# Optimization experiments

Hardware: AMD Instinct MI355X
Metric: run time of the kernel (lower is better)

The kernel has to match this reference:

```python
import jax, jax.numpy as jnp
import numpy as np

SCALE = 4.0  # InputEmbedding scale
D = 16       # coordinate dim (InputEmbedding input_dim)


def _p(k, shape, s=0.05):
    return jax.random.normal(k, shape, dtype=jnp.float32) * s


def setup_inputs() -> dict:
    key = jax.random.key(0)
    ks = jax.random.split(key, 20)
    T, N, E, H = 8, 2048, 256, 768
    return {
        "observed": jax.random.normal(ks[0], (T, N, D), dtype=jnp.float32),
        "emb_W": _p(ks[1], (E, D)), "emb_b": _p(ks[2], (E,)),
        "e1_Wih": _p(ks[3], (3 * H, E)), "e1_Whh": _p(ks[4], (3 * H, H)),
        "e1_bih": _p(ks[5], (3 * H,)), "e1_bhh": _p(ks[6], (3 * H,)),
        "e2_Wih": _p(ks[7], (3 * H, E + H)), "e2_Whh": _p(ks[8], (3 * H, H)),
        "e2_bih": _p(ks[9], (3 * H,)), "e2_bhh": _p(ks[10], (3 * H,)),
        "dec_Wih": _p(ks[11], (3 * H, E)), "dec_Whh": _p(ks[12], (3 * H, H)),
        "dec_bih": _p(ks[13], (3 * H,)), "dec_bhh": _p(ks[14], (3 * H,)),
        "h2n_W": _p(ks[15], (5, H)), "h2n_b": _p(ks[16], (5,)),
        "mix_W": _p(ks[17], (D, 5)), "mix_b": _p(ks[18], (D,)),
        "n_predict": 12,
    }


def _gru(x, h, Wih, Whh, bih, bhh):
    # torch.nn.GRUCell math
    gi = x @ Wih.T + bih          # [N, 3H]
    gh = h @ Whh.T + bhh          # [N, 3H]
    ir, iz, in_ = jnp.split(gi, 3, axis=-1)
    hr, hz, hn = jnp.split(gh, 3, axis=-1)
    r = jax.nn.sigmoid(ir + hr)
    z = jax.nn.sigmoid(iz + hz)
    n = jnp.tanh(in_ + r * hn)
    return (1.0 - z) * n + z * h


def reference(observed, emb_W, emb_b,
              e1_Wih, e1_Whh, e1_bih, e1_bhh,
              e2_Wih, e2_Whh, e2_bih, e2_bhh,
              dec_Wih, dec_Whh, dec_bih, dec_bhh,
              h2n_W, h2n_b, mix_W, mix_b, n_predict):
    T, N, _ = observed.shape
    H = e1_Whh.shape[1]
    embed = lambda v: (SCALE * v) @ emb_W.T + emb_b   # InputEmbedding
    h0 = jnp.zeros((N, H), observed.dtype)

    # --- backward (inverse-time) encoder1 pass ---
    inv = observed[::-1]
    vel_b = inv[:-1] - inv[1:]          # obs2 - obs1 on reversed sequence, [T-1, N, D]
    def step1(h, v):
        return _gru(embed(v), h, e1_Wih, e1_Whh, e1_bih, e1_bhh), None
    h_inv, _ = jax.lax.scan(step1, h0, vel_b)
    # NOTE: original mutates the python hidden_state list in place, so every
    # h_invs entry aliases the FINAL encoder1 state -> h_inv is constant over t.

    # --- forward encoder2 pass (input = [embed(vel), h_inv]) ---
    vel_f = observed[1:] - observed[:-1]   # [T-1, N, D]
    def step2(h, v):
        x = jnp.concatenate([embed(v), h_inv], axis=1)
        return _gru(x, h, e2_Wih, e2_Whh, e2_bih, e2_bhh), None
    h, _ = jax.lax.scan(step2, h0, vel_f)

    def h2n(hs):
        # Hidden2Normal: linear then constrain sigmas / correlation
        n = hs @ h2n_W.T + h2n_b
        return jnp.concatenate(
            [n[:, :2], 0.01 + 0.2 * jax.nn.softplus(n[:, 2:4]), 0.7 * jnp.tanh(n[:, 4:5])],
            axis=1)

    def dec_step(h, obs1, obs2):
        h = _gru(embed(obs2 - obs1), h, dec_Wih, dec_Whh, dec_bih, dec_bhh)
        normal = h2n(h)                                   # [N, 5]
        pos = obs2 + jax.nn.relu(normal @ mix_W.T + mix_b)  # mix: Linear(5 -> 16)
        return h, normal, pos

    # decoder step i=0: (observed[-2], observed[-1]); i=1: (observed[-1], positions[-1].detach())
    h, n0, p0 = dec_step(h, observed[-2], observed[-1])
    h, n1, p1 = dec_step(h, observed[-1], jax.lax.stop_gradient(p0))

    def scan_step(carry, _):
        h, pm2, pm1 = carry
        h, n, p = dec_step(h, jax.lax.stop_gradient(pm2), jax.lax.stop_gradient(pm1))
        return (h, pm1, p), (n, p)
    _, (ns, ps) = jax.lax.scan(scan_step, (h, p0, p1), None, length=n_predict - 2)

    rel_pred_scene = jnp.concatenate([jnp.stack([n0, n1]), ns], axis=0)  # [n_predict, N, 5]
    pred_scene = jnp.concatenate([jnp.stack([p0, p1]), ps], axis=0)      # [n_predict, N, 16]
    return rel_pred_scene, pred_scene
```

## Files before the change

### kernel.cpp

```cpp
#include <hip/hip_runtime.h>
#include <hip/hip_bf16.h>
#include <math.h>

#define H 768
#define NB 2048
#define DD 16

typedef __attribute__((ext_vector_type(8))) short bf16x8;
typedef __attribute__((ext_vector_type(4))) float f32x4;

__device__ __forceinline__ void gload_lds16(const void* g, void* lds) {
  __builtin_amdgcn_global_load_lds((const __attribute__((address_space(1))) void*)g,
                                   (__attribute__((address_space(3))) void*)lds, 16, 0, 0);
}
__device__ __forceinline__ float b2f(short s) {
  union { unsigned int u; float f; } c;
  c.u = ((unsigned int)(unsigned short)s) << 16;
  return c.f;
}
__device__ __forceinline__ short f2bs(float f) {
  __hip_bfloat16 h = __float2bfloat16(f);
  return *(short*)&h;
}

__global__ void k_m1(const float* __restrict__ e1W, const float* __restrict__ e2W,
                     const float* __restrict__ dW, const float* __restrict__ embW,
                     float* __restrict__ M1) {
  int idx = blockIdx.x * 256 + threadIdx.x;
  if (idx >= 3 * 2304 * 16) return;
  int d = idx & 15, g = (idx >> 4) % 2304, s = idx / (2304 * 16);
  const float* W = s == 0 ? e1W : s == 1 ? e2W : dW;
  int ld = s == 1 ? 1024 : 256;
  float sum = 0.f;
  for (int e = 0; e < 256; ++e) sum += W[(size_t)g * ld + e] * embW[e * 16 + d];
  M1[idx] = 4.0f * sum;
}

__global__ void k_biasP(const float* __restrict__ e1W, const float* __restrict__ e2W,
                        const float* __restrict__ dW, const float* __restrict__ embB,
                        const float* b1i, const float* b1h, const float* b2i, const float* b2h,
                        const float* b3i, const float* b3h, float* __restrict__ out) {
  int idx = blockIdx.x * 256 + threadIdx.x;
  if (idx >= 3 * 3072) return;
  int c = idx % 3072, s = idx / 3072;
  int f = (c >> 4) & 3, u = (c >> 6) * 16 + (c & 15);
  const float* W = s == 0 ? e1W : s == 1 ? e2W : dW;
  int ld = s == 1 ? 1024 : 256;
  const float* bi = s == 0 ? b1i : s == 1 ? b2i : b3i;
  const float* bh = s == 0 ? b1h : s == 1 ? b2h : b3h;
  float v;
  if (f == 3) {
    v = bh[1536 + u];
  } else {
    int g = (f < 2 ? f * 768 : 1536) + u;
    float acc = bi[g] + (f < 2 ? bh[g] : 0.f);
    for (int e = 0; e < 256; ++e) acc += W[(size_t)g * ld + e] * embB[e];
    v = acc;
  }
  out[idx] = v;
}

__global__ void k_packB3(const float* __restrict__ W1, const float* __restrict__ W2,
                         const float* __restrict__ W3, const float* __restrict__ M1all,
                         __hip_bfloat16* __restrict__ B1, __hip_bfloat16* __restrict__ B2,
                         __hip_bfloat16* __restrict__ B3) {
  int idx = blockIdx.x * 256 + threadIdx.x;
  if (idx >= 3072 * 800) return;
  int s = blockIdx.y;
  const float* Whh = s == 0 ? W1 : s == 1 ? W2 : W3;
  const float* M1s = M1all + (size_t)s * 2304 * 16;
  __hip_bfloat16* Bp = s == 0 ? B1 : s == 1 ? B2 : B3;
  int k = idx % 800, c = idx / 800;
  int f = (c >> 4) & 3, u = (c >> 6) * 16 + (c & 15);
  float v = 0.f;
  if (k < 768) {
    if (f == 0) v = Whh[(size_t)u * 768 + k];
    else if (f == 1) v = Whh[(size_t)(768 + u) * 768 + k];
    else if (f == 3) v = Whh[(size_t)(1536 + u) * 768 + k];
  } else if (k < 784) {
    if (f < 3) v = M1s[(size_t)(f * 768 + u) * 16 + (k - 768)];
  }
  Bp[idx] = __float2bfloat16(v);
}

__global__ void k_packB2g(const float* __restrict__ e2W, __hip_bfloat16* __restrict__ B2g) {
  int idx = blockIdx.x * 256 + threadIdx.x;
  if (idx >= 3072 * 768) return;
  int k = idx % 768, c = idx / 768;
  int f = (c >> 4) & 3, u = (c >> 6) * 16 + (c & 15);
  float v = (f < 3) ? e2W[(size_t)(f * 768 + u) * 1024 + 256 + k] : 0.f;
  B2g[idx] = __float2bfloat16(v);
}

__global__ void k_vel(const float* __restrict__ obs, __hip_bfloat16* __restrict__ velall) {
  int idx = blockIdx.x * 256 + threadIdx.x;
  if (idx >= 7 * 2048 * 32) return;
  int d = idx & 31, n = (idx >> 5) & 2047, s = idx >> 16;
  float v = 0.f;
  if (d < 16)
    v = obs[((size_t)(s + 1) * NB + n) * DD + d] - obs[((size_t)s * NB + n) * DD + d];
  velall[idx] = __float2bfloat16(v);
}

__global__ __launch_bounds__(256) void k_plain(
    const __hip_bfloat16* __restrict__ A, const __hip_bfloat16* __restrict__ B,
    __hip_bfloat16* __restrict__ C, int ldc) {
  __shared__ __align__(16) __hip_bfloat16 Asm[128 * 32];
  __shared__ __align__(16) __hip_bfloat16 Bsm[128 * 32];
  const int tid = threadIdx.x;
  const int w = tid >> 6, l = tid & 63;
  const int bm = blockIdx.y, bn = blockIdx.x;
  const int wm = w >> 1, wn = w & 1;
  const int lr = l & 15, lk = l >> 4;
  const int ks = (((tid & 3) ^ ((tid >> 3) & 3)) << 3);
  const int lks = ((lk ^ ((lr >> 1) & 3)) << 3);
  f32x4 acc[4][4];
#pragma unroll
  for (int m = 0; m < 4; ++m)
#pragma unroll
    for (int n = 0; n < 4; ++n) acc[m][n] = (f32x4){0.f, 0.f, 0.f, 0.f};
  const int rowA = bm * 128, rowB = bn * 128;
  const int rA = tid >> 2;
  for (int kb = 0; kb < H; kb += 32) {
#pragma unroll
    for (int i = 0; i < 2; ++i) {
      int r = i * 64 + rA;
      gload_lds16(A + (size_t)(rowA + r) * H + kb + ks, (char*)Asm + i * 4096 + w * 1024);
      gload_lds16(B + (size_t)(rowB + r) * H + kb + ks, (char*)Bsm + i * 4096 + w * 1024);
    }
    __syncthreads();
    bf16x8 af[4], bfr[4];
#pragma unroll
    for (int m = 0; m < 4; ++m)
      af[m] = *(const bf16x8*)(Asm + (wm * 64 + m * 16 + lr) * 32 + lks);
#pragma unroll
    for (int n = 0; n < 4; ++n)
      bfr[n] = *(const bf16x8*)(Bsm + (wn * 64 + n * 16 + lr) * 32 + lks);
#pragma unroll
    for (int m = 0; m < 4; ++m)
#pragma unroll
      for (int n = 0; n < 4; ++n)
        acc[m][n] = __builtin_amdgcn_mfma_f32_16x16x32_bf16(af[m], bfr[n], acc[m][n], 0, 0, 0);
    __syncthreads();
  }
#pragma unroll
  for (int m = 0; m < 4; ++m)
#pragma unroll
    for (int n = 0; n < 4; ++n) {
      int col = bn * 128 + wn * 64 + n * 16 + lr;
#pragma unroll
      for (int r4 = 0; r4 < 4; ++r4) {
        int row = rowA + wm * 64 + m * 16 + lk * 4 + r4;
        C[(size_t)row * ldc + col] = __float2bfloat16(acc[m][n][r4]);
      }
    }
}

__global__ __launch_bounds__(256) void k_step(
    const __hip_bfloat16* __restrict__ hin,
    const __hip_bfloat16* __restrict__ vel,
    const __hip_bfloat16* __restrict__ Bp,
    const float* __restrict__ bias,
    const __hip_bfloat16* __restrict__ g2a,
    __hip_bfloat16* __restrict__ hout) {
  __shared__ __align__(16) char lds[49152];
  const int tid = threadIdx.x;
  const int w = tid >> 6, l = tid & 63;
  const int nt = blockIdx.x, bm = blockIdx.y;
  const int rowA = bm * 128, colB = nt * 64;
  const int lr = l & 15, lk = l >> 4;
  const int wbase = w * 1024;
  const int rA = tid >> 2;
  const int ce = (((tid & 3) ^ ((tid >> 3) & 3)) << 3);
  const int lks = ((lk ^ ((lr >> 1) & 3)) << 3);

  auto STAGE = [&](int buf, int kb) {
#pragma unroll
    for (int i_ = 0; i_ < 2; ++i_) {
      int r_ = i_ * 64 + rA;
      const __hip_bfloat16* s_ = (kb < 768)
          ? hin + (size_t)(rowA + r_) * H + kb + ce
          : vel + (size_t)(rowA + r_) * 32 + ce;
      gload_lds16(s_, lds + buf * 12288 + i_ * 4096 + wbase);
    }
    gload_lds16(Bp + (size_t)(colB + rA) * 800 + kb + ce, lds + buf * 12288 + 8192 + wbase);
  };

  f32x4 acc[2][4];
#pragma unroll
  for (int m = 0; m < 2; ++m)
#pragma unroll
    for (int n = 0; n < 4; ++n) acc[m][n] = (f32x4){0.f, 0.f, 0.f, 0.f};

  STAGE(0, 0);
  STAGE(1, 32);
  STAGE(2, 64);

#pragma unroll
  for (int ki = 0; ki < 25; ++ki) {
    if (ki < 23)      asm volatile("s_waitcnt vmcnt(6)" ::: "memory");
    else if (ki == 23) asm volatile("s_waitcnt vmcnt(3)" ::: "memory");
    else               asm volatile("s_waitcnt vmcnt(0)" ::: "memory");
    __builtin_amdgcn_sched_barrier(0);
    __builtin_amdgcn_s_barrier();
    __builtin_amdgcn_sched_barrier(0);
    if (ki < 22) STAGE((ki + 3) & 3, (ki + 3) * 32);
    const char* cur = lds + (ki & 3) * 12288;
    const __hip_bfloat16* Ab = (const __hip_bfloat16*)cur;
    const __hip_bfloat16* Bb = (const __hip_bfloat16*)(cur + 8192);
    bf16x8 a0 = *(const bf16x8*)(Ab + (w * 32 + lr) * 32 + lks);
    bf16x8 a1 = *(const bf16x8*)(Ab + (w * 32 + 16 + lr) * 32 + lks);
    bf16x8 b0 = *(const bf16x8*)(Bb + lr * 32 + lks);
    bf16x8 b1 = *(const bf16x8*)(Bb + (16 + lr) * 32 + lks);
    const bool last = (ki == 24);
    bf16x8 b2 = *(const bf16x8*)(Bb + ((last ? 32 : 48) + lr) * 32 + lks);
    __builtin_amdgcn_s_setprio(1);
    acc[0][0] = __builtin_amdgcn_mfma_f32_16x16x32_bf16(a0, b0, acc[0][0], 0, 0, 0);
    acc[1][0] = __builtin_amdgcn_mfma_f32_16x16x32_bf16(a1, b0, acc[1][0], 0, 0, 0);
    acc[0][1] = __builtin_amdgcn_mfma_f32_16x16x32_bf16(a0, b1, acc[0][1], 0, 0, 0);
    acc[1][1] = __builtin_amdgcn_mfma_f32_16x16x32_bf16(a1, b1, acc[1][1], 0, 0, 0);
    if (last) {
      acc[0][2] = __builtin_amdgcn_mfma_f32_16x16x32_bf16(a0, b2, acc[0][2], 0, 0, 0);
      acc[1][2] = __builtin_amdgcn_mfma_f32_16x16x32_bf16(a1, b2, acc[1][2], 0, 0, 0);
    } else {
      acc[0][3] = __builtin_amdgcn_mfma_f32_16x16x32_bf16(a0, b2, acc[0][3], 0, 0, 0);
      acc[1][3] = __builtin_amdgcn_mfma_f32_16x16x32_bf16(a1, b2, acc[1][3], 0, 0, 0);
    }
    __builtin_amdgcn_s_setprio(0);
  }

  __syncthreads();
  short* T = (short*)lds;
  const float* bp = bias + nt * 64;
#pragma unroll
  for (int n = 0; n < 4; ++n) {
    float bv = bp[n * 16 + lr];
#pragma unroll
    for (int m = 0; m < 2; ++m) {
      int rbase = w * 32 + m * 16 + lk * 4;
#pragma unroll
      for (int r4 = 0; r4 < 4; ++r4)
        T[(rbase + r4) * 72 + n * 16 + lr] = f2bs(acc[m][n][r4] + bv);
    }
  }
  __syncthreads();

  const int row = tid >> 1;
  const int ub = (tid & 1) * 8;
  const size_t grow = (size_t)(rowA + row);
  const short* Tp = T + row * 72;
  bf16x8 Lr = *(const bf16x8*)(Tp + ub);
  bf16x8 Lz = *(const bf16x8*)(Tp + 16 + ub);
  bf16x8 Li = *(const bf16x8*)(Tp + 32 + ub);
  bf16x8 Lh = *(const bf16x8*)(Tp + 48 + ub);
  bf16x8 h8 = *(const bf16x8*)(hin + grow * H + nt * 16 + ub);
  bf16x8 gr, gz, gi_;
  if (g2a) {
    const __hip_bfloat16* gp = g2a + grow * 3072 + nt * 64;
    gr  = *(const bf16x8*)(gp + ub);
    gz  = *(const bf16x8*)(gp + 16 + ub);
    gi_ = *(const bf16x8*)(gp + 32 + ub);
  }
  union { bf16x8 v; short s[8]; } ob;
#pragma unroll
  for (int e = 0; e < 8; ++e) {
    float xr = b2f(Lr[e]), xz = b2f(Lz[e]), xi = b2f(Li[e]), xh = b2f(Lh[e]);
    if (g2a) { xr += b2f(gr[e]); xz += b2f(gz[e]); xi += b2f(gi_[e]); }
    float r = 1.f / (1.f + expf(-xr));
    float z = 1.f / (1.f + expf(-xz));
    float nn = tanhf(xi + r * xh);
    float hv = (1.f - z) * nn + z * b2f(h8[e]);
    ob.s[e] = f2bs(hv);
  }
  *(bf16x8*)(hout + grow * H + nt * 16 + ub) = ob.v;
}

__global__ void k_head(const __hip_bfloat16* __restrict__ h, const float* __restrict__ obs2,
                       const float* __restrict__ h2n_W, const float* __restrict__ h2n_b,
                       const float* __restrict__ mix_W, const float* __restrict__ mix_b,
                       float* __restrict__ rel_out, float* __restrict__ pos_out,
                       __hip_bfloat16* __restrict__ velout) {
  int wv = threadIdx.x >> 6, lane = threadIdx.x & 63;
  int row = blockIdx.x * 4 + wv;
  float s0 = 0.f, s1 = 0.f, s2 = 0.f, s3 = 0.f, s4 = 0.f;
  for (int k = lane; k < H; k += 64) {
    float hv = b2f(((const short*)h)[(size_t)row * H + k]);
    s0 += hv * h2n_W[k];
    s1 += hv * h2n_W[H + k];
    s2 += hv * h2n_W[2 * H + k];
    s3 += hv * h2n_W[3 * H + k];
    s4 += hv * h2n_W[4 * H + k];
  }
#pragma unroll
  for (int off = 32; off; off >>= 1) {
    s0 += __shfl_down(s0, off);
    s1 += __shfl_down(s1, off);
    s2 += __shfl_down(s2, off);
    s3 += __shfl_down(s3, off);
    s4 += __shfl_down(s4, off);
  }
  s0 = __shfl(s0, 0); s1 = __shfl(s1, 0); s2 = __shfl(s2, 0);
  s3 = __shfl(s3, 0); s4 = __shfl(s4, 0);
  float n0 = s0 + h2n_b[0], n1 = s1 + h2n_b[1];
  float x2 = s2 + h2n_b[2], x3 = s3 + h2n_b[3], x4 = s4 + h2n_b[4];
  float n2 = 0.01f + 0.2f * (x2 > 0.f ? x2 + log1pf(expf(-x2)) : log1pf(expf(x2)));
  float n3 = 0.01f + 0.2f * (x3 > 0.f ? x3 + log1pf(expf(-x3)) : log1pf(expf(x3)));
  float n4 = 0.7f * tanhf(x4);
  float rl = 0.f;
  if (lane < DD) {
    float a = mix_b[lane] + n0 * mix_W[lane * 5 + 0] + n1 * mix_W[lane * 5 + 1] +
              n2 * mix_W[lane * 5 + 2] + n3 * mix_W[lane * 5 + 3] + n4 * mix_W[lane * 5 + 4];
    rl = a > 0.f ? a : 0.f;
    pos_out[(size_t)row * DD + lane] = obs2[(size_t)row * DD + lane] + rl;
  }
  if (lane < 32)
    velout[(size_t)row * 32 + lane] = __float2bfloat16(lane < DD ? rl : 0.f);
  if (lane == 0) {
    rel_out[(size_t)row * 5 + 0] = n0;
    rel_out[(size_t)row * 5 + 1] = n1;
    rel_out[(size_t)row * 5 + 2] = n2;
    rel_out[(size_t)row * 5 + 3] = n3;
    rel_out[(size_t)row * 5 + 4] = n4;
  }
}

extern "C" void kernel_launch(void* const* d_in, const int* in_sizes, int n_in,
                              void* d_out, int out_size, void* d_ws, size_t ws_size,
                              hipStream_t stream) {
  (void)in_sizes; (void)n_in; (void)out_size; (void)ws_size;
  const float* observed = (const float*)d_in[0];
  const float* emb_W   = (const float*)d_in[1];
  const float* emb_b   = (const float*)d_in[2];
  const float* e1_Wih  = (const float*)d_in[3];
  const float* e1_Whh  = (const float*)d_in[4];
  const float* e1_bih  = (const float*)d_in[5];
  const float* e1_bhh  = (const float*)d_in[6];
  const float* e2_Wih  = (const float*)d_in[7];
  const float* e2_Whh  = (const float*)d_in[8];
  const float* e2_bih  = (const float*)d_in[9];
  const float* e2_bhh  = (const float*)d_in[10];
  const float* dec_Wih = (const float*)d_in[11];
  const float* dec_Whh = (const float*)d_in[12];
  const float* dec_bih = (const float*)d_in[13];
  const float* dec_bhh = (const float*)d_in[14];
  const float* h2n_W   = (const float*)d_in[15];
  const float* h2n_b   = (const float*)d_in[16];
  const float* mix_W   = (const float*)d_in[17];
  const float* mix_b   = (const float*)d_in[18];

  char* p = (char*)d_ws;
  auto alloc = [&](size_t bytes) { char* r = p; p += (bytes + 255) & ~(size_t)255; return r; };

  __hip_bfloat16* hz     = (__hip_bfloat16*)alloc((size_t)NB * H * 2);
  __hip_bfloat16* hp0    = (__hip_bfloat16*)alloc((size_t)NB * H * 2);
  __hip_bfloat16* hp1    = (__hip_bfloat16*)alloc((size_t)NB * H * 2);
  __hip_bfloat16* velall = (__hip_bfloat16*)alloc((size_t)7 * NB * 32 * 2);
  __hip_bfloat16* dvel   = (__hip_bfloat16*)alloc((size_t)NB * 32 * 2);
  __hip_bfloat16* Bp1    = (__hip_bfloat16*)alloc((size_t)3072 * 800 * 2);
  __hip_bfloat16* Bp2    = (__hip_bfloat16*)alloc((size_t)3072 * 800 * 2);
  __hip_bfloat16* Bp3    = (__hip_bfloat16*)alloc((size_t)3072 * 800 * 2);
  __hip_bfloat16* B2g    = (__hip_bfloat16*)alloc((size_t)3072 * 768 * 2);
  __hip_bfloat16* g2add  = (__hip_bfloat16*)alloc((size_t)NB * 3072 * 2);
  float*          M1     = (float*)alloc((size_t)3 * 2304 * 16 * 4);
  float*          biasP  = (float*)alloc((size_t)3 * 3072 * 4);

  hipMemsetAsync(hz, 0, (size_t)NB * H * 2, stream);
  k_m1<<<(3 * 2304 * 16 + 255) / 256, 256, 0, stream>>>(e1_Wih, e2_Wih, dec_Wih, emb_W, M1);
  k_biasP<<<(3 * 3072 + 255) / 256, 256, 0, stream>>>(e1_Wih, e2_Wih, dec_Wih, emb_b,
                                                      e1_bih, e1_bhh, e2_bih, e2_bhh,
                                                      dec_bih, dec_bhh, biasP);
  k_packB3<<<dim3((3072 * 800 + 255) / 256, 3), 256, 0, stream>>>(e1_Whh, e2_Whh, dec_Whh,
                                                                  M1, Bp1, Bp2, Bp3);
  k_packB2g<<<(3072 * 768 + 255) / 256, 256, 0, stream>>>(e2_Wih, B2g);
  k_vel<<<(7 * NB * 32 + 255) / 256, 256, 0, stream>>>(observed, velall);

  dim3 gs(48, 16);
  const __hip_bfloat16* src;
  __hip_bfloat16* dst = hp0;

  src = hz;
  for (int t = 0; t < 7; ++t) {
    k_step<<<gs, 256, 0, stream>>>(src, velall + (size_t)(6 - t) * NB * 32, Bp1, biasP,
                                   nullptr, dst);
    src = dst;
    dst = (dst == hp0) ? hp1 : hp0;
  }
  k_plain<<<dim3(24, 16), 256, 0, stream>>>(src, B2g, g2add, 3072);

  src = hz;
  for (int t = 0; t < 7; ++t) {
    k_step<<<gs, 256, 0, stream>>>(src, velall + (size_t)t * NB * 32, Bp2, biasP + 3072,
                                   g2add, dst);
    src = dst;
    dst = (dst == hp0) ? hp1 : hp0;
  }

  float* rel  = (float*)d_out;
  float* pred = (float*)d_out + (size_t)12 * NB * 5;
  for (int k = 0; k < 12; ++k) {
    const __hip_bfloat16* vk = (k == 0) ? velall + (size_t)6 * NB * 32 : dvel;
    k_step<<<gs, 256, 0, stream>>>(src, vk, Bp3, biasP + 2 * 3072, nullptr, dst);
    const float* o2 = (k == 0) ? observed + (size_t)7 * NB * DD
                               : pred + (size_t)(k - 1) * NB * DD;
    k_head<<<NB / 4, 256, 0, stream>>>(dst, o2, h2n_W, h2n_b, mix_W, mix_b,
                                       rel + (size_t)k * NB * 5, pred + (size_t)k * NB * DD,
                                       dvel);
    src = dst;
    dst = (dst == hp0) ? hp1 : hp0;
  }
}
```

Before: 773.3 us.

## Fuse decoder head into GRU step kernel and skip zero-state matmul

The decoder output head (h2n, softplus/tanh, mix, relu) for step j is now computed at the start of the next GRU step kernel. Its velocity result is written straight into LDS as the extra K-slice, so the separate head launches and the dvel round-trip go away. First steps with zero hidden state skip the 768-wide recurrent GEMM and use only the velocity tile. The pipeline drops from 4 to 3 LDS stages, launch bounds ask for 3 blocks per SM, and the prep kernels are merged into fewer launches. The cost is that every one of the 48 column blocks recomputes the head dot product over 768 elements per row, which is redundant work.

```diff
diff --git a/kernel.cpp b/kernel.cpp
--- a/kernel.cpp
+++ b/kernel.cpp
@@ -5,6 +5,7 @@
 #define H 768
 #define NB 2048
 #define DD 16
+#define VELOFF 36864
 
 typedef __attribute__((ext_vector_type(8))) short bf16x8;
 typedef __attribute__((ext_vector_type(4))) float f32x4;
@@ -23,52 +24,59 @@
   return *(short*)&h;
 }
 
-__global__ void k_m1(const float* __restrict__ e1W, const float* __restrict__ e2W,
-                     const float* __restrict__ dW, const float* __restrict__ embW,
-                     float* __restrict__ M1) {
-  int idx = blockIdx.x * 256 + threadIdx.x;
-  if (idx >= 3 * 2304 * 16) return;
-  int d = idx & 15, g = (idx >> 4) % 2304, s = idx / (2304 * 16);
-  const float* W = s == 0 ? e1W : s == 1 ? e2W : dW;
-  int ld = s == 1 ? 1024 : 256;
-  float sum = 0.f;
-  for (int e = 0; e < 256; ++e) sum += W[(size_t)g * ld + e] * embW[e * 16 + d];
-  M1[idx] = 4.0f * sum;
-}
-
-__global__ void k_biasP(const float* __restrict__ e1W, const float* __restrict__ e2W,
-                        const float* __restrict__ dW, const float* __restrict__ embB,
-                        const float* b1i, const float* b1h, const float* b2i, const float* b2h,
-                        const float* b3i, const float* b3h, float* __restrict__ out) {
-  int idx = blockIdx.x * 256 + threadIdx.x;
-  if (idx >= 3 * 3072) return;
-  int c = idx % 3072, s = idx / 3072;
-  int f = (c >> 4) & 3, u = (c >> 6) * 16 + (c & 15);
-  const float* W = s == 0 ? e1W : s == 1 ? e2W : dW;
-  int ld = s == 1 ? 1024 : 256;
-  const float* bi = s == 0 ? b1i : s == 1 ? b2i : b3i;
-  const float* bh = s == 0 ? b1h : s == 1 ? b2h : b3h;
-  float v;
-  if (f == 3) {
-    v = bh[1536 + u];
-  } else {
-    int g = (f < 2 ? f * 768 : 1536) + u;
-    float acc = bi[g] + (f < 2 ? bh[g] : 0.f);
-    for (int e = 0; e < 256; ++e) acc += W[(size_t)g * ld + e] * embB[e];
-    v = acc;
-  }
-  out[idx] = v;
-}
-
-__global__ void k_packB3(const float* __restrict__ W1, const float* __restrict__ W2,
-                         const float* __restrict__ W3, const float* __restrict__ M1all,
+__global__ void k_prep(const float* __restrict__ e1W, const float* __restrict__ e2W,
+                       const float* __restrict__ dW, const float* __restrict__ embB,
+                       const float* b1i, const float* b1h, const float* b2i, const float* b2h,
+                       const float* b3i, const float* b3h, const float* __restrict__ obs,
+                       float* __restrict__ biasP, __hip_bfloat16* __restrict__ B2g,
+                       __hip_bfloat16* __restrict__ velall) {
+  const int stride = gridDim.x * 256;
+  const int gt = blockIdx.x * 256 + threadIdx.x;
+  for (int idx = gt; idx < 3 * 3072; idx += stride) {
+    int c = idx % 3072, s = idx / 3072;
+    int f = (c >> 4) & 3, u = (c >> 6) * 16 + (c & 15);
+    const float* W = s == 0 ? e1W : s == 1 ? e2W : dW;
+    int ld = s == 1 ? 1024 : 256;
+    const float* bi = s == 0 ? b1i : s == 1 ? b2i : b3i;
+    const float* bh = s == 0 ? b1h : s == 1 ? b2h : b3h;
+    float v;
+    if (f == 3) {
+      v = bh[1536 + u];
+    } else {
+      int g = (f < 2 ? f * 768 : 1536) + u;
+      float acc = bi[g] + (f < 2 ? bh[g] : 0.f);
+      for (int e = 0; e < 256; ++e) acc += W[(size_t)g * ld + e] * embB[e];
+      v = acc;
+    }
+    biasP[idx] = v;
+  }
+  for (int idx = gt; idx < 3072 * 768; idx += stride) {
+    int k = idx % 768, c = idx / 768;
+    int f = (c >> 4) & 3, u = (c >> 6) * 16 + (c & 15);
+    float v = (f < 3) ? e2W[(size_t)(f * 768 + u) * 1024 + 256 + k] : 0.f;
+    B2g[idx] = __float2bfloat16(v);
+  }
+  for (int idx = gt; idx < 7 * 2048 * 32; idx += stride) {
+    int d = idx & 31, n = (idx >> 5) & 2047, s = idx >> 16;
+    float v = 0.f;
+    if (d < 16)
+      v = obs[((size_t)(s + 1) * NB + n) * DD + d] - obs[((size_t)s * NB + n) * DD + d];
+    velall[idx] = __float2bfloat16(v);
+  }
+}
+
+__global__ void k_packB3(const float* __restrict__ W1h, const float* __restrict__ W2h,
+                         const float* __restrict__ W3h, const float* __restrict__ W1i,
+                         const float* __restrict__ W2i, const float* __restrict__ W3i,
+                         const float* __restrict__ embW,
                          __hip_bfloat16* __restrict__ B1, __hip_bfloat16* __restrict__ B2,
                          __hip_bfloat16* __restrict__ B3) {
   int idx = blockIdx.x * 256 + threadIdx.x;
   if (idx >= 3072 * 800) return;
   int s = blockIdx.y;
-  const float* Whh = s == 0 ? W1 : s == 1 ? W2 : W3;
-  const float* M1s = M1all + (size_t)s * 2304 * 16;
+  const float* Whh = s == 0 ? W1h : s == 1 ? W2h : W3h;
+  const float* Wih = s == 0 ? W1i : s == 1 ? W2i : W3i;
+  int ldih = s == 1 ? 1024 : 256;
   __hip_bfloat16* Bp = s == 0 ? B1 : s == 1 ? B2 : B3;
   int k = idx % 800, c = idx / 800;
   int f = (c >> 4) & 3, u = (c >> 6) * 16 + (c & 15);
@@ -77,29 +85,14 @@
     if (f == 0) v = Whh[(size_t)u * 768 + k];
     else if (f == 1) v = Whh[(size_t)(768 + u) * 768 + k];
     else if (f == 3) v = Whh[(size_t)(1536 + u) * 768 + k];
-  } else if (k < 784) {
-    if (f < 3) v = M1s[(size_t)(f * 768 + u) * 16 + (k - 768)];
+  } else if (k < 784 && f < 3) {
+    int g = (f < 2 ? f * 768 : 1536) + u;
+    float acc = 0.f;
+    int d = k - 768;
+    for (int e = 0; e < 256; ++e) acc += Wih[(size_t)g * ldih + e] * embW[e * 16 + d];
+    v = 4.0f * acc;
   }
   Bp[idx] = __float2bfloat16(v);
-}
-
-__global__ void k_packB2g(const float* __restrict__ e2W, __hip_bfloat16* __restrict__ B2g) {
-  int idx = blockIdx.x * 256 + threadIdx.x;
-  if (idx >= 3072 * 768) return;
-  int k = idx % 768, c = idx / 768;
-  int f = (c >> 4) & 3, u = (c >> 6) * 16 + (c & 15);
-  float v = (f < 3) ? e2W[(size_t)(f * 768 + u) * 1024 + 256 + k] : 0.f;
-  B2g[idx] = __float2bfloat16(v);
-}
-
-__global__ void k_vel(const float* __restrict__ obs, __hip_bfloat16* __restrict__ velall) {
-  int idx = blockIdx.x * 256 + threadIdx.x;
-  if (idx >= 7 * 2048 * 32) return;
-  int d = idx & 31, n = (idx >> 5) & 2047, s = idx >> 16;
-  float v = 0.f;
-  if (d < 16)
-    v = obs[((size_t)(s + 1) * NB + n) * DD + d] - obs[((size_t)s * NB + n) * DD + d];
-  velall[idx] = __float2bfloat16(v);
 }
 
 __global__ __launch_bounds__(256) void k_plain(
@@ -156,85 +149,159 @@
     }
 }
 
-__global__ __launch_bounds__(256) void k_step(
+template <int MODE>
+__global__ __launch_bounds__(256, 3) void k_step(
     const __hip_bfloat16* __restrict__ hin,
     const __hip_bfloat16* __restrict__ vel,
     const __hip_bfloat16* __restrict__ Bp,
     const float* __restrict__ bias,
     const __hip_bfloat16* __restrict__ g2a,
-    __hip_bfloat16* __restrict__ hout) {
-  __shared__ __align__(16) char lds[49152];
+    __hip_bfloat16* __restrict__ hout,
+    const float* __restrict__ h2n_W, const float* __restrict__ h2n_b,
+    const float* __restrict__ mix_W, const float* __restrict__ mix_b,
+    const float* __restrict__ o2,
+    float* __restrict__ rel_out, float* __restrict__ pos_out) {
+  __shared__ __align__(16) char lds[45056];
   const int tid = threadIdx.x;
   const int w = tid >> 6, l = tid & 63;
   const int nt = blockIdx.x, bm = blockIdx.y;
   const int rowA = bm * 128, colB = nt * 64;
   const int lr = l & 15, lk = l >> 4;
-  const int wbase = w * 1024;
-  const int rA = tid >> 2;
+  const int rS = tid >> 2;
   const int ce = (((tid & 3) ^ ((tid >> 3) & 3)) << 3);
   const int lks = ((lk ^ ((lr >> 1) & 3)) << 3);
+  const int wbase = w * 1024;
 
   auto STAGE = [&](int buf, int kb) {
 #pragma unroll
-    for (int i_ = 0; i_ < 2; ++i_) {
-      int r_ = i_ * 64 + rA;
-      const __hip_bfloat16* s_ = (kb < 768)
-          ? hin + (size_t)(rowA + r_) * H + kb + ce
-          : vel + (size_t)(rowA + r_) * 32 + ce;
-      gload_lds16(s_, lds + buf * 12288 + i_ * 4096 + wbase);
-    }
-    gload_lds16(Bp + (size_t)(colB + rA) * 800 + kb + ce, lds + buf * 12288 + 8192 + wbase);
+    for (int i_ = 0; i_ < 2; ++i_)
+      gload_lds16(hin + (size_t)(rowA + i_ * 64 + rS) * H + kb + ce,
+                  lds + buf * 12288 + i_ * 4096 + wbase);
+    gload_lds16(Bp + (size_t)(colB + rS) * 800 + kb + ce, lds + buf * 12288 + 8192 + wbase);
   };
 
+  if (MODE == 0) {
+#pragma unroll
+    for (int i_ = 0; i_ < 2; ++i_)
+      gload_lds16(vel + (size_t)(rowA + i_ * 64 + rS) * 32 + ce,
+                  lds + VELOFF + i_ * 4096 + wbase);
+  }
+  if (hin) { STAGE(0, 0); STAGE(1, 32); }
+  else     gload_lds16(Bp + (size_t)(colB + rS) * 800 + 768 + ce, lds + 8192 + wbase);
+
+  if (MODE == 1) {
+    const int hr = tid >> 1, p = tid & 1;
+    const short* hrow = (const short*)hin + (size_t)(rowA + hr) * H + p * 384;
+    float s0 = 0.f, s1 = 0.f, s2 = 0.f, s3 = 0.f, s4 = 0.f;
+    for (int kk = 0; kk < 384; kk += 8) {
+      bf16x8 h8 = *(const bf16x8*)(hrow + kk);
+#pragma unroll
+      for (int e = 0; e < 8; ++e) {
+        float hv = b2f(h8[e]);
+        int k2 = p * 384 + kk + e;
+        s0 += hv * h2n_W[k2];
+        s1 += hv * h2n_W[768 + k2];
+        s2 += hv * h2n_W[1536 + k2];
+        s3 += hv * h2n_W[2304 + k2];
+        s4 += hv * h2n_W[3072 + k2];
+      }
+    }
+    s0 += __shfl_xor(s0, 1); s1 += __shfl_xor(s1, 1); s2 += __shfl_xor(s2, 1);
+    s3 += __shfl_xor(s3, 1); s4 += __shfl_xor(s4, 1);
+    float n0 = s0 + h2n_b[0], n1 = s1 + h2n_b[1];
+    float x2 = s2 + h2n_b[2], x3 = s3 + h2n_b[3], x4 = s4 + h2n_b[4];
+    float n2 = 0.01f + 0.2f * (x2 > 0.f ? x2 + log1pf(expf(-x2)) : log1pf(expf(x2)));
+    float n3 = 0.01f + 0.2f * (x3 > 0.f ? x3 + log1pf(expf(-x3)) : log1pf(expf(x3)));
+    float n4 = 0.7f * tanhf(x4);
+    union { bf16x8 v; short s[8]; } pk;
+#pragma unroll
+    for (int e = 0; e < 8; ++e) {
+      int d = p * 8 + e;
+      float a = mix_b[d] + n0 * mix_W[d * 5 + 0] + n1 * mix_W[d * 5 + 1] +
+                n2 * mix_W[d * 5 + 2] + n3 * mix_W[d * 5 + 3] + n4 * mix_W[d * 5 + 4];
+      float rl = fmaxf(a, 0.f);
+      pk.s[e] = f2bs(rl);
+      if (nt == 0)
+        pos_out[(size_t)(rowA + hr) * DD + d] = o2[(size_t)(rowA + hr) * DD + d] + rl;
+    }
+    if (nt == 0 && p == 0) {
+      float* rp = rel_out + (size_t)(rowA + hr) * 5;
+      rp[0] = n0; rp[1] = n1; rp[2] = n2; rp[3] = n3; rp[4] = n4;
+    }
+    int swz = (hr >> 1) & 3;
+    *(bf16x8*)(lds + VELOFF + hr * 64 + ((p ^ swz) << 4)) = pk.v;
+    bf16x8 z8 = {};
+    *(bf16x8*)(lds + VELOFF + hr * 64 + (((2 + p) ^ swz) << 4)) = z8;
+    asm volatile("s_waitcnt lgkmcnt(0)" ::: "memory");
+    __builtin_amdgcn_s_barrier();
+  }
+
   f32x4 acc[2][4];
 #pragma unroll
   for (int m = 0; m < 2; ++m)
 #pragma unroll
     for (int n = 0; n < 4; ++n) acc[m][n] = (f32x4){0.f, 0.f, 0.f, 0.f};
 
-  STAGE(0, 0);
-  STAGE(1, 32);
-  STAGE(2, 64);
-
-#pragma unroll
-  for (int ki = 0; ki < 25; ++ki) {
-    if (ki < 23)      asm volatile("s_waitcnt vmcnt(6)" ::: "memory");
-    else if (ki == 23) asm volatile("s_waitcnt vmcnt(3)" ::: "memory");
-    else               asm volatile("s_waitcnt vmcnt(0)" ::: "memory");
+  if (hin) {
+#pragma unroll
+    for (int ki = 0; ki < 25; ++ki) {
+      if (ki <= 22)      asm volatile("s_waitcnt vmcnt(3)" ::: "memory");
+      else if (ki == 23) asm volatile("s_waitcnt vmcnt(1)" ::: "memory");
+      else               asm volatile("s_waitcnt vmcnt(0)" ::: "memory");
+      __builtin_amdgcn_sched_barrier(0);
+      __builtin_amdgcn_s_barrier();
+      __builtin_amdgcn_sched_barrier(0);
+      if (ki < 22) STAGE((ki + 2) % 3, (ki + 2) * 32);
+      else if (ki == 22)
+        gload_lds16(Bp + (size_t)(colB + rS) * 800 + 768 + ce, lds + 8192 + wbase);
+      const bool last = (ki == 24);
+      const __hip_bfloat16* Ab = last ? (const __hip_bfloat16*)(lds + VELOFF)
+                                      : (const __hip_bfloat16*)(lds + (ki % 3) * 12288);
+      const __hip_bfloat16* Bb = (const __hip_bfloat16*)(lds + (ki % 3) * 12288 + 8192);
+      bf16x8 a0 = *(const bf16x8*)(Ab + (w * 32 + lr) * 32 + lks);
+      bf16x8 a1 = *(const bf16x8*)(Ab + (w * 32 + 16 + lr) * 32 + lks);
+      bf16x8 b0 = *(const bf16x8*)(Bb + lr * 32 + lks);
+      bf16x8 b1 = *(const bf16x8*)(Bb + (16 + lr) * 32 + lks);
+      bf16x8 b2 = *(const bf16x8*)(Bb + ((last ? 32 : 48) + lr) * 32 + lks);
+      __builtin_amdgcn_s_setprio(1);
+      acc[0][0] = __builtin_amdgcn_mfma_f32_16x16x32_bf16(a0, b0, acc[0][0], 0, 0, 0);
+      acc[1][0] = __builtin_amdgcn_mfma_f32_16x16x32_bf16(a1, b0, acc[1][0], 0, 0, 0);
+      acc[0][1] = __builtin_amdgcn_mfma_f32_16x16x32_bf16(a0, b1, acc[0][1], 0, 0, 0);
+      acc[1][1] = __builtin_amdgcn_mfma_f32_16x16x32_bf16(a1, b1, acc[1][1], 0, 0, 0);
+      if (last) {
+        acc[0][2] = __builtin_amdgcn_mfma_f32_16x16x32_bf16(a0, b2, acc[0][2], 0, 0, 0);
+        acc[1][2] = __builtin_amdgcn_mfma_f32_16x16x32_bf16(a1, b2, acc[1][2], 0, 0, 0);
+      } else {
+        acc[0][3] = __builtin_amdgcn_mfma_f32_16x16x32_bf16(a0, b2, acc[0][3], 0, 0, 0);
+        acc[1][3] = __builtin_amdgcn_mfma_f32_16x16x32_bf16(a1, b2, acc[1][3], 0, 0, 0);
+      }
+      __builtin_amdgcn_s_setprio(0);
+    }
+  } else {
+    asm volatile("s_waitcnt vmcnt(0)" ::: "memory");
     __builtin_amdgcn_sched_barrier(0);
     __builtin_amdgcn_s_barrier();
     __builtin_amdgcn_sched_barrier(0);
-    if (ki < 22) STAGE((ki + 3) & 3, (ki + 3) * 32);
-    const char* cur = lds + (ki & 3) * 12288;
-    const __hip_bfloat16* Ab = (const __hip_bfloat16*)cur;
-    const __hip_bfloat16* Bb = (const __hip_bfloat16*)(cur + 8192);
+    const __hip_bfloat16* Ab = (const __hip_bfloat16*)(lds + VELOFF);
+    const __hip_bfloat16* Bb = (const __hip_bfloat16*)(lds + 8192);
     bf16x8 a0 = *(const bf16x8*)(Ab + (w * 32 + lr) * 32 + lks);
     bf16x8 a1 = *(const bf16x8*)(Ab + (w * 32 + 16 + lr) * 32 + lks);
     bf16x8 b0 = *(const bf16x8*)(Bb + lr * 32 + lks);
     bf16x8 b1 = *(const bf16x8*)(Bb + (16 + lr) * 32 + lks);
-    const bool last = (ki == 24);
-    bf16x8 b2 = *(const bf16x8*)(Bb + ((last ? 32 : 48) + lr) * 32 + lks);
-    __builtin_amdgcn_s_setprio(1);
+    bf16x8 b2 = *(const bf16x8*)(Bb + (32 + lr) * 32 + lks);
     acc[0][0] = __builtin_amdgcn_mfma_f32_16x16x32_bf16(a0, b0, acc[0][0], 0, 0, 0);
     acc[1][0] = __builtin_amdgcn_mfma_f32_16x16x32_bf16(a1, b0, acc[1][0], 0, 0, 0);
     acc[0][1] = __builtin_amdgcn_mfma_f32_16x16x32_bf16(a0, b1, acc[0][1], 0, 0, 0);
     acc[1][1] = __builtin_amdgcn_mfma_f32_16x16x32_bf16(a1, b1, acc[1][1], 0, 0, 0);
-    if (last) {
-      acc[0][2] = __builtin_amdgcn_mfma_f32_16x16x32_bf16(a0, b2, acc[0][2], 0, 0, 0);
-      acc[1][2] = __builtin_amdgcn_mfma_f32_16x16x32_bf16(a1, b2, acc[1][2], 0, 0, 0);
-    } else {
-      acc[0][3] = __builtin_amdgcn_mfma_f32_16x16x32_bf16(a0, b2, acc[0][3], 0, 0, 0);
-      acc[1][3] = __builtin_amdgcn_mfma_f32_16x16x32_bf16(a1, b2, acc[1][3], 0, 0, 0);
-    }
-    __builtin_amdgcn_s_setprio(0);
+    acc[0][2] = __builtin_amdgcn_mfma_f32_16x16x32_bf16(a0, b2, acc[0][2], 0, 0, 0);
+    acc[1][2] = __builtin_amdgcn_mfma_f32_16x16x32_bf16(a1, b2, acc[1][2], 0, 0, 0);
   }
 
   __syncthreads();
   short* T = (short*)lds;
-  const float* bp = bias + nt * 64;
 #pragma unroll
   for (int n = 0; n < 4; ++n) {
-    float bv = bp[n * 16 + lr];
+    float bv = bias[colB + n * 16 + lr];
 #pragma unroll
     for (int m = 0; m < 2; ++m) {
       int rbase = w * 32 + m * 16 + lk * 4;
@@ -253,10 +320,11 @@
   bf16x8 Lz = *(const bf16x8*)(Tp + 16 + ub);
   bf16x8 Li = *(const bf16x8*)(Tp + 32 + ub);
   bf16x8 Lh = *(const bf16x8*)(Tp + 48 + ub);
-  bf16x8 h8 = *(const bf16x8*)(hin + grow * H + nt * 16 + ub);
-  bf16x8 gr, gz, gi_;
+  bf16x8 h8 = {};
+  if (hin) h8 = *(const bf16x8*)(hin + grow * H + nt * 16 + ub);
+  bf16x8 gr = {}, gz = {}, gi_ = {};
   if (g2a) {
-    const __hip_bfloat16* gp = g2a + grow * 3072 + nt * 64;
+    const __hip_bfloat16* gp = g2a + grow * 3072 + colB;
     gr  = *(const bf16x8*)(gp + ub);
     gz  = *(const bf16x8*)(gp + 16 + ub);
     gi_ = *(const bf16x8*)(gp + 32 + ub);
@@ -269,17 +337,16 @@
     float r = 1.f / (1.f + expf(-xr));
     float z = 1.f / (1.f + expf(-xz));
     float nn = tanhf(xi + r * xh);
-    float hv = (1.f - z) * nn + z * b2f(h8[e]);
+    float hv = hin ? ((1.f - z) * nn + z * b2f(h8[e])) : ((1.f - z) * nn);
     ob.s[e] = f2bs(hv);
   }
   *(bf16x8*)(hout + grow * H + nt * 16 + ub) = ob.v;
 }
 
-__global__ void k_head(const __hip_bfloat16* __restrict__ h, const float* __restrict__ obs2,
-                       const float* __restrict__ h2n_W, const float* __restrict__ h2n_b,
-                       const float* __restrict__ mix_W, const float* __restrict__ mix_b,
-                       float* __restrict__ rel_out, float* __restrict__ pos_out,
-                       __hip_bfloat16* __restrict__ velout) {
+__global__ void k_headF(const __hip_bfloat16* __restrict__ h, const float* __restrict__ obs2,
+                        const float* __restrict__ h2n_W, const float* __restrict__ h2n_b,
+                        const float* __restrict__ mix_W, const float* __restrict__ mix_b,
+                        float* __restrict__ rel_out, float* __restrict__ pos_out) {
   int wv = threadIdx.x >> 6, lane = threadIdx.x & 63;
   int row = blockIdx.x * 4 + wv;
   float s0 = 0.f, s1 = 0.f, s2 = 0.f, s3 = 0.f, s4 = 0.f;
@@ -306,15 +373,12 @@
   float n2 = 0.01f + 0.2f * (x2 > 0.f ? x2 + log1pf(expf(-x2)) : log1pf(expf(x2)));
   float n3 = 0.01f + 0.2f * (x3 > 0.f ? x3 + log1pf(expf(-x3)) : log1pf(expf(x3)));
   float n4 = 0.7f * tanhf(x4);
-  float rl = 0.f;
   if (lane < DD) {
     float a = mix_b[lane] + n0 * mix_W[lane * 5 + 0] + n1 * mix_W[lane * 5 + 1] +
               n2 * mix_W[lane * 5 + 2] + n3 * mix_W[lane * 5 + 3] + n4 * mix_W[lane * 5 + 4];
-    rl = a > 0.f ? a : 0.f;
+    float rl = a > 0.f ? a : 0.f;
     pos_out[(size_t)row * DD + lane] = obs2[(size_t)row * DD + lane] + rl;
   }
-  if (lane < 32)
-    velout[(size_t)row * 32 + lane] = __float2bfloat16(lane < DD ? rl : 0.f);
   if (lane == 0) {
     rel_out[(size_t)row * 5 + 0] = n0;
     rel_out[(size_t)row * 5 + 1] = n1;
@@ -351,61 +415,59 @@
   char* p = (char*)d_ws;
   auto alloc = [&](size_t bytes) { char* r = p; p += (bytes + 255) & ~(size_t)255; return r; };
 
-  __hip_bfloat16* hz     = (__hip_bfloat16*)alloc((size_t)NB * H * 2);
   __hip_bfloat16* hp0    = (__hip_bfloat16*)alloc((size_t)NB * H * 2);
   __hip_bfloat16* hp1    = (__hip_bfloat16*)alloc((size_t)NB * H * 2);
   __hip_bfloat16* velall = (__hip_bfloat16*)alloc((size_t)7 * NB * 32 * 2);
-  __hip_bfloat16* dvel   = (__hip_bfloat16*)alloc((size_t)NB * 32 * 2);
   __hip_bfloat16* Bp1    = (__hip_bfloat16*)alloc((size_t)3072 * 800 * 2);
   __hip_bfloat16* Bp2    = (__hip_bfloat16*)alloc((size_t)3072 * 800 * 2);
   __hip_bfloat16* Bp3    = (__hip_bfloat16*)alloc((size_t)3072 * 800 * 2);
   __hip_bfloat16* B2g    = (__hip_bfloat16*)alloc((size_t)3072 * 768 * 2);
   __hip_bfloat16* g2add  = (__hip_bfloat16*)alloc((size_t)NB * 3072 * 2);
-  float*          M1     = (float*)alloc((size_t)3 * 2304 * 16 * 4);
   float*          biasP  = (float*)alloc((size_t)3 * 3072 * 4);
 
-  hipMemsetAsync(hz, 0, (size_t)NB * H * 2, stream);
-  k_m1<<<(3 * 2304 * 16 + 255) / 256, 256, 0, stream>>>(e1_Wih, e2_Wih, dec_Wih, emb_W, M1);
-  k_biasP<<<(3 * 3072 + 255) / 256, 256, 0, stream>>>(e1_Wih, e2_Wih, dec_Wih, emb_b,
-                                                      e1_bih, e1_bhh, e2_bih, e2_bhh,
-                                                      dec_bih, dec_bhh, biasP);
-  k_packB3<<<dim3((3072 * 800 + 255) / 256, 3), 256, 0, stream>>>(e1_Whh, e2_Whh, dec_Whh,
-                                                                  M1, Bp1, Bp2, Bp3);
-  k_packB2g<<<(3072 * 768 + 255) / 256, 256, 0, stream>>>(e2_Wih, B2g);
-  k_vel<<<(7 * NB * 32 + 255) / 256, 256, 0, stream>>>(observed, velall);
+  k_prep<<<1024, 256, 0, stream>>>(e1_Wih, e2_Wih, dec_Wih, emb_b,
+                                   e1_bih, e1_bhh, e2_bih, e2_bhh, dec_bih, dec_bhh,
+                                   observed, biasP, B2g, velall);
+  k_packB3<<<dim3((3072 * 800 + 255) / 256, 3), 256, 0, stream>>>(
+      e1_Whh, e2_Whh, dec_Whh, e1_Wih, e2_Wih, dec_Wih, emb_W, Bp1, Bp2, Bp3);
 
   dim3 gs(48, 16);
-  const __hip_bfloat16* src;
-  __hip_bfloat16* dst = hp0;
-
-  src = hz;
-  for (int t = 0; t < 7; ++t) {
-    k_step<<<gs, 256, 0, stream>>>(src, velall + (size_t)(6 - t) * NB * 32, Bp1, biasP,
-                                   nullptr, dst);
-    src = dst;
-    dst = (dst == hp0) ? hp1 : hp0;
-  }
-  k_plain<<<dim3(24, 16), 256, 0, stream>>>(src, B2g, g2add, 3072);
-
-  src = hz;
-  for (int t = 0; t < 7; ++t) {
-    k_step<<<gs, 256, 0, stream>>>(src, velall + (size_t)t * NB * 32, Bp2, biasP + 3072,
-                                   g2add, dst);
-    src = dst;
-    dst = (dst == hp0) ? hp1 : hp0;
-  }
-
   float* rel  = (float*)d_out;
   float* pred = (float*)d_out + (size_t)12 * NB * 5;
-  for (int k = 0; k < 12; ++k) {
-    const __hip_bfloat16* vk = (k == 0) ? velall + (size_t)6 * NB * 32 : dvel;
-    k_step<<<gs, 256, 0, stream>>>(src, vk, Bp3, biasP + 2 * 3072, nullptr, dst);
-    const float* o2 = (k == 0) ? observed + (size_t)7 * NB * DD
-                               : pred + (size_t)(k - 1) * NB * DD;
-    k_head<<<NB / 4, 256, 0, stream>>>(dst, o2, h2n_W, h2n_b, mix_W, mix_b,
-                                       rel + (size_t)k * NB * 5, pred + (size_t)k * NB * DD,
-                                       dvel);
-    src = dst;
-    dst = (dst == hp0) ? hp1 : hp0;
-  }
-}
+  const __hip_bfloat16* src = nullptr;
+  __hip_bfloat16* dst = hp0;
+  auto flip = [&]() { src = dst; dst = (dst == hp0) ? hp1 : hp0; };
+
+  for (int t = 0; t < 7; ++t) {
+    k_step<0><<<gs, 256, 0, stream>>>(t == 0 ? nullptr : src,
+                                      velall + (size_t)(6 - t) * NB * 32, Bp1, biasP,
+                                      nullptr, dst, h2n_W, h2n_b, mix_W, mix_b,
+                                      nullptr, nullptr, nullptr);
+    flip();
+  }
+  k_plain<<<dim3(24, 16), 256, 0, stream>>>(src, B2g, g2add, 3072);
+
+  for (int t = 0; t < 7; ++t) {
+    k_step<0><<<gs, 256, 0, stream>>>(t == 0 ? nullptr : src,
+                                      velall + (size_t)t * NB * 32, Bp2, biasP + 3072,
+                                      g2add, dst, h2n_W, h2n_b, mix_W, mix_b,
+                                      nullptr, nullptr, nullptr);
+    flip();
+  }
+
+  k_step<0><<<gs, 256, 0, stream>>>(src, velall + (size_t)6 * NB * 32, Bp3, biasP + 6144,
+                                    nullptr, dst, h2n_W, h2n_b, mix_W, mix_b,
+                                    nullptr, nullptr, nullptr);
+  flip();
+  for (int j = 0; j <= 10; ++j) {
+    const float* o2 = (j == 0) ? observed + (size_t)7 * NB * DD
+                               : pred + (size_t)(j - 1) * NB * DD;
+    k_step<1><<<gs, 256, 0, stream>>>(src, nullptr, Bp3, biasP + 6144,
+                                      nullptr, dst, h2n_W, h2n_b, mix_W, mix_b,
+                                      o2, rel + (size_t)j * NB * 5, pred + (size_t)j * NB * DD);
+    flip();
+  }
+  k_headF<<<NB / 4, 256, 0, stream>>>(src, pred + (size_t)10 * NB * DD,
+                                      h2n_W, h2n_b, mix_W, mix_b,
+                                      rel + (size_t)11 * NB * 5, pred + (size_t)11 * NB * DD);
+}
```

Result: slower. 1.706 ms (+120.6%).
